# Kernel optimization log

Measured on AMD Instinct MI355X. Metric: run time of the kernel, lower is better.

Reference implementation:

```python
import jax, jax.numpy as jnp
import numpy as np

B, S, DIM = 1, 2048, 2048
NH, NKV, HD = 32, 8, 64
NREP = NH // NKV
SCALE = 1.0 / float(np.sqrt(HD))
NEG = -1e30


def _apply_rope(q, k, rope_cache):
    # q: (B,S,NH,HD), k: (B,S,NKV,HD); rope_cache: (S, HD) = [cos | sin], each HD//2 wide
    cos = rope_cache[:, : HD // 2][None, :, None, :]  # (1,S,1,HD/2)
    sin = rope_cache[:, HD // 2 :][None, :, None, :]

    def rot(x):
        x1, x2 = x[..., : HD // 2], x[..., HD // 2 :]
        return jnp.concatenate([x1 * cos - x2 * sin, x1 * sin + x2 * cos], axis=-1)

    return rot(q), rot(k)


def setup_inputs() -> dict:
    key = jax.random.key(0)
    ks = jax.random.split(key, 12)
    std = 0.02
    x = jax.random.normal(ks[0], (B, S, DIM), jnp.float32)
    # real rotary cos/sin cache
    inv_freq = 1.0 / (10000.0 ** (np.arange(0, HD, 2, dtype=np.float64) / HD))
    freqs = np.outer(np.arange(S, dtype=np.float64), inv_freq)
    rope_cache = jnp.asarray(
        np.concatenate([np.cos(freqs), np.sin(freqs)], axis=-1), jnp.float32
    )  # (S, HD)
    return {
        "x": x,
        "rope_cache": rope_cache,
        "wq_w": jax.random.normal(ks[1], (NH * HD, DIM), jnp.float32) * std,
        "wq_b": jax.random.normal(ks[2], (NH * HD,), jnp.float32) * std,
        "wk_w": jax.random.normal(ks[3], (NKV * HD, DIM), jnp.float32) * std,
        "wk_b": jax.random.normal(ks[4], (NKV * HD,), jnp.float32) * std,
        "wv_w": jax.random.normal(ks[5], (NKV * HD, DIM), jnp.float32) * std,
        "wv_b": jax.random.normal(ks[6], (NKV * HD,), jnp.float32) * std,
        "wo_w": jax.random.normal(ks[7], (DIM, NH * HD), jnp.float32) * std,
        "wo_b": jax.random.normal(ks[8], (DIM,), jnp.float32) * std,
        "sinks": jax.random.normal(ks[9], (NH,), jnp.float32) * std,
    }


def reference(x, rope_cache, wq_w, wq_b, wk_w, wk_b, wv_w, wv_b, wo_w, wo_b, sinks):
    q = (x @ wq_w.T + wq_b).reshape(B, S, NH, HD)
    k = (x @ wk_w.T + wk_b).reshape(B, S, NKV, HD)
    v = (x @ wv_w.T + wv_b).reshape(B, S, NKV, HD)
    q, k = _apply_rope(q, k, rope_cache)
    q = q.transpose(0, 2, 1, 3)  # (B,NH,S,HD)
    k = jnp.repeat(k.transpose(0, 2, 1, 3), NREP, axis=1)  # GQA expand -> (B,NH,S,HD)
    v = jnp.repeat(v.transpose(0, 2, 1, 3), NREP, axis=1)
    scores = jnp.einsum("bhqd,bhkd->bhqk", q, k) * SCALE
    causal = jnp.tril(jnp.ones((S, S), bool))
    scores = jnp.where(causal[None, None], scores, NEG)
    lse = jax.scipy.special.logsumexp(scores, axis=-1)  # (B,NH,S)
    attn = jnp.exp(scores - lse[..., None])
    out = jnp.einsum("bhqk,bhkd->bhqd", attn, v)
    sink_scale = jax.nn.sigmoid(lse - sinks[None, :, None])  # (B,NH,S)
    out = out * sink_scale[..., None]
    out = out.transpose(0, 2, 1, 3).reshape(B, S, NH * HD)
    return out @ wo_w.T + wo_b
```

## Files before the change

kernel.cpp:

```cpp
#include <hip/hip_runtime.h>

typedef unsigned short ushort_t;
typedef short s8v __attribute__((ext_vector_type(8)));
typedef float f4v __attribute__((ext_vector_type(4)));

#define DIMK   2048
#define NHEAD  32
#define HDIM   64
#define SCALE_LOG2E 0.18033688f

__device__ __forceinline__ unsigned short f2bf(float f) {
    unsigned u = __float_as_uint(f);
    u += 0x7fffu + ((u >> 16) & 1u);
    return (unsigned short)(u >> 16);
}

__device__ __forceinline__ unsigned pack_bf2(float f0, float f1) {
    unsigned a = __float_as_uint(f0) + 0x8000u;
    unsigned b = __float_as_uint(f1) + 0x8000u;
    return __builtin_amdgcn_perm(b, a, 0x07060302u);
}

__device__ __forceinline__ float fexp2(float x) {
#if __has_builtin(__builtin_amdgcn_exp2f)
    return __builtin_amdgcn_exp2f(x);
#else
    return exp2f(x);
#endif
}

__device__ __forceinline__ void gll16(const void* g, void* l) {
    __builtin_amdgcn_global_load_lds(
        (const __attribute__((address_space(1))) void*)g,
        (__attribute__((address_space(3))) void*)l, 16, 0, 0);
}

__device__ __forceinline__ f4v mfma16(s8v a, s8v b, f4v c) {
    return __builtin_amdgcn_mfma_f32_16x16x32_bf16(a, b, c, 0, 0, 0);
}

__global__ __launch_bounds__(256) void cast_all(
    const float* __restrict__ x,  const float* __restrict__ wq,
    const float* __restrict__ wk, const float* __restrict__ wv,
    const float* __restrict__ wo,
    ushort_t* __restrict__ xb,  ushort_t* __restrict__ wqb,
    ushort_t* __restrict__ wkb, ushort_t* __restrict__ wvb,
    ushort_t* __restrict__ wob)
{
    int i = blockIdx.x * 256 + threadIdx.x;
    const float* src; ushort_t* dst;
    if      (i < 1048576) { src = x;  dst = xb; }
    else if (i < 2097152) { src = wq; dst = wqb; i -= 1048576; }
    else if (i < 2359296) { src = wk; dst = wkb; i -= 2097152; }
    else if (i < 2621440) { src = wv; dst = wvb; i -= 2359296; }
    else                  { src = wo; dst = wob; i -= 2621440; }
    float4 v = ((const float4*)src)[i];
    ushort4 o;
    o.x = f2bf(v.x); o.y = f2bf(v.y); o.z = f2bf(v.z); o.w = f2bf(v.w);
    ((ushort4*)dst)[i] = o;
}

__device__ __forceinline__ void gemm_core64(
    const ushort_t* __restrict__ A, const ushort_t* __restrict__ Bt,
    int bm, int bn64, ushort_t* As, ushort_t* Bs, f4v acc[2][4])
{
    const int tid  = threadIdx.x;
    const int wave = tid >> 6, lane = tid & 63;
    const int c = lane & 15, q4 = lane >> 4;

    const ushort_t* ag = A  + (size_t)(bm * 128 + wave * 32 + (lane >> 2)) * DIMK + (lane & 3) * 8;
    const ushort_t* bg = Bt + (size_t)(bn64 * 64 + wave * 16 + (lane >> 2)) * DIMK + (lane & 3) * 8;
    ushort_t* as0 = As + (wave * 32) * 32;
    ushort_t* as1 = As + (wave * 32 + 16) * 32;
    ushort_t* bs0 = Bs + (wave * 16) * 32;

    for (int k0 = 0; k0 < DIMK; k0 += 32) {
        gll16(ag + k0,             as0);
        gll16(ag + 16 * DIMK + k0, as1);
        gll16(bg + k0,             bs0);
        __syncthreads();
        s8v af[2], bfv[4];
#pragma unroll
        for (int mt = 0; mt < 2; ++mt)
            af[mt] = *(const s8v*)(As + (wave * 32 + mt * 16 + c) * 32 + q4 * 8);
#pragma unroll
        for (int nt = 0; nt < 4; ++nt)
            bfv[nt] = *(const s8v*)(Bs + (nt * 16 + c) * 32 + q4 * 8);
#pragma unroll
        for (int mt = 0; mt < 2; ++mt)
#pragma unroll
            for (int nt = 0; nt < 4; ++nt)
                acc[mt][nt] = mfma16(af[mt], bfv[nt], acc[mt][nt]);
        __syncthreads();
    }
}

__global__ __launch_bounds__(256) void qkv_gemm(
    const ushort_t* __restrict__ Xb,
    const ushort_t* __restrict__ Wqb, const ushort_t* __restrict__ Wkb, const ushort_t* __restrict__ Wvb,
    const float* __restrict__ biasq, const float* __restrict__ biask, const float* __restrict__ biasv,
    const float* __restrict__ rope,
    ushort_t* __restrict__ Qo, ushort_t* __restrict__ Kblk, ushort_t* __restrict__ Vblk)
{
    __shared__ ushort_t As[128 * 32], Bs[64 * 32];
    const int nb = blockIdx.x, bm = blockIdx.y;
    const ushort_t* Bt; const float* bias; int nbl, mode;
    if      (nb < 32) { Bt = Wqb; bias = biasq; nbl = nb;      mode = 0; }
    else if (nb < 40) { Bt = Wkb; bias = biask; nbl = nb - 32; mode = 1; }
    else              { Bt = Wvb; bias = biasv; nbl = nb - 40; mode = 2; }

    const f4v fz = {0.f, 0.f, 0.f, 0.f};
    f4v acc[2][4];
    for (int i = 0; i < 2; ++i) for (int j = 0; j < 4; ++j) acc[i][j] = fz;

    gemm_core64(Xb, Bt, bm, nbl, As, Bs, acc);

    const int tid = threadIdx.x, wave = tid >> 6, lane = tid & 63;
    const int c = lane & 15, q4 = lane >> 4;

    if (mode == 0) {
#pragma unroll
        for (int mt = 0; mt < 2; ++mt)
#pragma unroll
            for (int r = 0; r < 4; ++r) {
                int row = bm * 128 + wave * 32 + mt * 16 + q4 * 4 + r;
                const float* rp = rope + row * 64;
#pragma unroll
                for (int nt = 0; nt < 2; ++nt) {
                    int d   = nt * 16 + c;
                    int col = nbl * 64 + d;
                    float cs = rp[d], sn = rp[32 + d];
                    float x1 = acc[mt][nt][r]     + bias[col];
                    float x2 = acc[mt][nt + 2][r] + bias[col + 32];
                    Qo[(size_t)row * 2048 + col]      = f2bf((x1 * cs - x2 * sn) * SCALE_LOG2E);
                    Qo[(size_t)row * 2048 + col + 32] = f2bf((x1 * sn + x2 * cs) * SCALE_LOG2E);
                }
            }
    } else if (mode == 1) {
#pragma unroll
        for (int mt = 0; mt < 2; ++mt)
#pragma unroll
            for (int r = 0; r < 4; ++r) {
                int row = bm * 128 + wave * 32 + mt * 16 + q4 * 4 + r;
                const float* rp = rope + row * 64;
                int kt = row >> 6, ntk = (row & 63) >> 4, ck = row & 15;
#pragma unroll
                for (int nt = 0; nt < 2; ++nt) {
                    int d   = nt * 16 + c;
                    int col = nbl * 64 + d;
                    float cs = rp[d], sn = rp[32 + d];
                    float x1 = acc[mt][nt][r]     + bias[col];
                    float x2 = acc[mt][nt + 2][r] + bias[col + 32];
                    float o1 = x1 * cs - x2 * sn;
                    float o2 = x1 * sn + x2 * cs;
                    {   int dd = d;       int kc = dd >> 5, q4k = (dd >> 3) & 3, j = dd & 7;
                        Kblk[(((((size_t)nbl * 32 + kt) * 2 + kc) * 4 + ntk) * 64 + q4k * 16 + ck) * 8 + j] = f2bf(o1); }
                    {   int dd = d + 32;  int kc = dd >> 5, q4k = (dd >> 3) & 3, j = dd & 7;
                        Kblk[(((((size_t)nbl * 32 + kt) * 2 + kc) * 4 + ntk) * 64 + q4k * 16 + ck) * 8 + j] = f2bf(o2); }
                }
            }
    } else {
#pragma unroll
        for (int mt = 0; mt < 2; ++mt)
#pragma unroll
            for (int nt = 0; nt < 4; ++nt)
#pragma unroll
                for (int r = 0; r < 4; ++r) {
                    int row = bm * 128 + wave * 32 + mt * 16 + q4 * 4 + r;
                    int col = nbl * 64 + nt * 16 + c;
                    int kt = row >> 6, K64 = row & 63;
                    int kp = (K64 & 15) * 4 + (K64 >> 4);
                    int kc = kp >> 5, q4v = (kp >> 3) & 3, j = kp & 7;
                    Vblk[(((((size_t)nbl * 32 + kt) * 2 + kc) * 4 + nt) * 64 + q4v * 16 + c) * 8 + j]
                        = f2bf(acc[mt][nt][r] + bias[col]);
                }
    }
}

__global__ __launch_bounds__(256) void proj_gemm(
    const ushort_t* __restrict__ Ob, const ushort_t* __restrict__ Wob,
    const float* __restrict__ bias, float* __restrict__ Co)
{
    __shared__ ushort_t As[128 * 32], Bs[64 * 32];
    const f4v fz = {0.f, 0.f, 0.f, 0.f};
    f4v acc[2][4];
    for (int i = 0; i < 2; ++i) for (int j = 0; j < 4; ++j) acc[i][j] = fz;

    gemm_core64(Ob, Wob, blockIdx.y, blockIdx.x, As, Bs, acc);

    const int tid = threadIdx.x, wave = tid >> 6, lane = tid & 63;
    const int c = lane & 15, q4 = lane >> 4;
#pragma unroll
    for (int mt = 0; mt < 2; ++mt)
#pragma unroll
        for (int nt = 0; nt < 4; ++nt)
#pragma unroll
            for (int r = 0; r < 4; ++r) {
                int row = blockIdx.y * 128 + wave * 32 + mt * 16 + q4 * 4 + r;
                int col = blockIdx.x * 64 + nt * 16 + c;
                Co[(size_t)row * 2048 + col] = acc[mt][nt][r] + bias[col];
            }
}

__global__ __launch_bounds__(256) void attn_kernel(
    const ushort_t* __restrict__ Qb,
    const ushort_t* __restrict__ Kblk,
    const ushort_t* __restrict__ Vblk,
    const float* __restrict__ sinks,
    ushort_t* __restrict__ Ob)
{
    __shared__ ushort_t Ps[4][32 * 72];
    const int p = blockIdx.x, h = blockIdx.y, kvh = h >> 2;
    const int tid = threadIdx.x, wave = tid >> 6, lane = tid & 63;
    const int c = lane & 15, q4 = lane >> 4;
    const int t  = (wave < 2) ? p : (31 - p);
    const int q0 = t * 64 + (wave & 1) * 32;
    ushort_t* Pw = &Ps[wave][0];

    s8v qf[2][2];
#pragma unroll
    for (int mi = 0; mi < 2; ++mi)
#pragma unroll
        for (int kc = 0; kc < 2; ++kc)
            qf[mi][kc] = *(const s8v*)(Qb + (size_t)(q0 + mi * 16 + c) * 2048 + h * 64 + kc * 32 + q4 * 8);

    const f4v fz = {0.f, 0.f, 0.f, 0.f};
    f4v Oacc[2][4];
    float Lp[2][4];
#pragma unroll
    for (int mi = 0; mi < 2; ++mi) {
#pragma unroll
        for (int dt = 0; dt < 4; ++dt) Oacc[mi][dt] = fz;
#pragma unroll
        for (int r = 0; r < 4; ++r) Lp[mi][r] = 0.f;
    }

    const ushort_t* kbase = Kblk + (size_t)kvh * 32 * 4096;
    const ushort_t* vbase = Vblk + (size_t)kvh * 32 * 4096;

    s8v kfA[4][2], vfA[4][2], kfB[4][2], vfB[4][2];

#define ATTN_PF(KF, VF, KT)                                                      \
    do {                                                                         \
        const ushort_t* kp_ = kbase + (size_t)(KT) * 4096;                       \
        const ushort_t* vp_ = vbase + (size_t)(KT) * 4096;                       \
        _Pragma("unroll")                                                        \
        for (int kc = 0; kc < 2; ++kc) {                                         \
            _Pragma("unroll")                                                    \
            for (int nt = 0; nt < 4; ++nt) {                                     \
                KF[nt][kc] = *(const s8v*)(kp_ + ((kc * 4 + nt) * 64 + lane) * 8);\
                VF[nt][kc] = *(const s8v*)(vp_ + ((kc * 4 + nt) * 64 + lane) * 8);\
            }                                                                    \
        }                                                                        \
    } while (0)

#define ATTN_BODY(KF, VF, KT)                                                    \
    do {                                                                         \
        f4v S[2][4];                                                             \
        _Pragma("unroll")                                                        \
        for (int mi = 0; mi < 2; ++mi) {                                         \
            _Pragma("unroll")                                                    \
            for (int nt = 0; nt < 4; ++nt) S[mi][nt] = fz;                       \
        }                                                                        \
        _Pragma("unroll")                                                        \
        for (int kc = 0; kc < 2; ++kc) {                                         \
            _Pragma("unroll")                                                    \
            for (int nt = 0; nt < 4; ++nt) {                                     \
                _Pragma("unroll")                                                \
                for (int mi = 0; mi < 2; ++mi)                                   \
                    S[mi][nt] = mfma16(qf[mi][kc], KF[nt][kc], S[mi][nt]);       \
            }                                                                    \
        }                                                                        \
        if ((KT) == t) {                                                         \
            _Pragma("unroll")                                                    \
            for (int mi = 0; mi < 2; ++mi) {                                     \
                _Pragma("unroll")                                                \
                for (int nt = 0; nt < 4; ++nt) {                                 \
                    int key = t * 64 + nt * 16 + c;                              \
                    _Pragma("unroll")                                            \
                    for (int r = 0; r < 4; ++r) {                                \
                        int qrow = q0 + mi * 16 + q4 * 4 + r;                    \
                        if (key > qrow) S[mi][nt][r] = -1.0e30f;                 \
                    }                                                            \
                }                                                                \
            }                                                                    \
        }                                                                        \
        _Pragma("unroll")                                                        \
        for (int mi = 0; mi < 2; ++mi) {                                         \
            _Pragma("unroll")                                                    \
            for (int r = 0; r < 4; ++r) {                                        \
                float p0 = fexp2(S[mi][0][r]), p1 = fexp2(S[mi][1][r]);          \
                float p2 = fexp2(S[mi][2][r]), p3 = fexp2(S[mi][3][r]);          \
                Lp[mi][r] += (p0 + p1) + (p2 + p3);                              \
                int2 w_; w_.x = (int)pack_bf2(p0, p1); w_.y = (int)pack_bf2(p2, p3); \
                *(int2*)(Pw + (mi * 16 + q4 * 4 + r) * 72 + c * 4) = w_;         \
            }                                                                    \
        }                                                                        \
        s8v pa[2][2];                                                            \
        _Pragma("unroll")                                                        \
        for (int mi = 0; mi < 2; ++mi) {                                         \
            _Pragma("unroll")                                                    \
            for (int kc = 0; kc < 2; ++kc)                                       \
                pa[mi][kc] = *(const s8v*)(Pw + (mi * 16 + c) * 72 + kc * 32 + q4 * 8); \
        }                                                                        \
        _Pragma("unroll")                                                        \
        for (int kc = 0; kc < 2; ++kc) {                                         \
            _Pragma("unroll")                                                    \
            for (int dt = 0; dt < 4; ++dt) {                                     \
                _Pragma("unroll")                                                \
                for (int mi = 0; mi < 2; ++mi)                                   \
                    Oacc[mi][dt] = mfma16(pa[mi][kc], VF[dt][kc], Oacc[mi][dt]); \
            }                                                                    \
        }                                                                        \
    } while (0)

    ATTN_PF(kfA, vfA, 0);
    int kt = 0;
    while (true) {
        int n1 = (kt + 1 <= t) ? kt + 1 : t;
        ATTN_PF(kfB, vfB, n1);
        ATTN_BODY(kfA, vfA, kt);
        ++kt; if (kt > t) break;
        int n2 = (kt + 1 <= t) ? kt + 1 : t;
        ATTN_PF(kfA, vfA, n2);
        ATTN_BODY(kfB, vfB, kt);
        ++kt; if (kt > t) break;
    }
#undef ATTN_PF
#undef ATTN_BODY

#pragma unroll
    for (int mi = 0; mi < 2; ++mi)
#pragma unroll
        for (int r = 0; r < 4; ++r)
#pragma unroll
            for (int off = 1; off < 16; off <<= 1)
                Lp[mi][r] += __shfl_xor(Lp[mi][r], off);

    const float sk = sinks[h];
#pragma unroll
    for (int mi = 0; mi < 2; ++mi)
#pragma unroll
        for (int r = 0; r < 4; ++r) {
            float L = Lp[mi][r];
            float lse = __logf(L);
            float sig = 1.f / (1.f + __expf(sk - lse));
            float sc  = sig / L;
            int row = q0 + mi * 16 + q4 * 4 + r;
#pragma unroll
            for (int dt = 0; dt < 4; ++dt)
                Ob[(size_t)row * 2048 + h * 64 + dt * 16 + c] = f2bf(Oacc[mi][dt][r] * sc);
        }
}

extern "C" void kernel_launch(void* const* d_in, const int* in_sizes, int n_in,
                              void* d_out, int out_size, void* d_ws, size_t ws_size,
                              hipStream_t stream)
{
    (void)in_sizes; (void)n_in; (void)out_size; (void)ws_size;
    const float* x     = (const float*)d_in[0];
    const float* rope  = (const float*)d_in[1];
    const float* wq    = (const float*)d_in[2];
    const float* qb    = (const float*)d_in[3];
    const float* wk    = (const float*)d_in[4];
    const float* kb    = (const float*)d_in[5];
    const float* wv    = (const float*)d_in[6];
    const float* vb    = (const float*)d_in[7];
    const float* wo    = (const float*)d_in[8];
    const float* wob_f = (const float*)d_in[9];
    const float* sinks = (const float*)d_in[10];
    float* out = (float*)d_out;

    char* ws = (char*)d_ws;
    ushort_t* xb   = (ushort_t*)(ws);
    ushort_t* wqb  = (ushort_t*)(ws + (8ull  << 20));
    ushort_t* wkb  = (ushort_t*)(ws + (16ull << 20));
    ushort_t* wvb  = (ushort_t*)(ws + (18ull << 20));
    ushort_t* wob  = (ushort_t*)(ws + (20ull << 20));
    ushort_t* qo   = (ushort_t*)(ws + (28ull << 20));
    ushort_t* kblk = (ushort_t*)(ws + (36ull << 20));
    ushort_t* vblk = (ushort_t*)(ws + (38ull << 20));
    ushort_t* ao   = (ushort_t*)(ws + (40ull << 20));

    cast_all<<<14336, 256, 0, stream>>>(x, wq, wk, wv, wo, xb, wqb, wkb, wvb, wob);
    qkv_gemm<<<dim3(48, 16), 256, 0, stream>>>(xb, wqb, wkb, wvb, qb, kb, vb, rope, qo, kblk, vblk);
    attn_kernel<<<dim3(16, 32), 256, 0, stream>>>(qo, kblk, vblk, sinks, ao);
    proj_gemm<<<dim3(32, 16), 256, 0, stream>>>(ao, wob, wob_f, out);
}
```

Before: 258.5 us.

## Split attention into one 64-row query tile per block with 16-row waves

The attention kernel now launches one block per 64-row query tile (32x32 grid, heaviest tiles first) instead of pairing a light and a heavy tile per block. Each wave now owns 16 query rows instead of 32. The explicit double-buffered K/V register prefetch is replaced by a simple loop that loads K/V each iteration. This gives more blocks and lower register use per wave, aiming for better occupancy and load balance. In exchange, K/V fragments are reused across fewer query rows, so K/V traffic per query rises and latency hiding now depends on occupancy rather than the software prefetch.

New measurement: 265.0 us. +2.5%, slower.

```diff
diff --git a/kernel.cpp b/kernel.cpp
--- a/kernel.cpp
+++ b/kernel.cpp
@@ -209,148 +209,99 @@
     const float* __restrict__ sinks,
     ushort_t* __restrict__ Ob)
 {
-    __shared__ ushort_t Ps[4][32 * 72];
-    const int p = blockIdx.x, h = blockIdx.y, kvh = h >> 2;
+    __shared__ ushort_t Ps[4][16 * 72];
+    const int t = 31 - blockIdx.x, h = blockIdx.y, kvh = h >> 2;
     const int tid = threadIdx.x, wave = tid >> 6, lane = tid & 63;
     const int c = lane & 15, q4 = lane >> 4;
-    const int t  = (wave < 2) ? p : (31 - p);
-    const int q0 = t * 64 + (wave & 1) * 32;
+    const int q0 = t * 64 + wave * 16;
     ushort_t* Pw = &Ps[wave][0];
 
-    s8v qf[2][2];
-#pragma unroll
-    for (int mi = 0; mi < 2; ++mi)
-#pragma unroll
-        for (int kc = 0; kc < 2; ++kc)
-            qf[mi][kc] = *(const s8v*)(Qb + (size_t)(q0 + mi * 16 + c) * 2048 + h * 64 + kc * 32 + q4 * 8);
+    s8v qf[2];
+#pragma unroll
+    for (int kc = 0; kc < 2; ++kc)
+        qf[kc] = *(const s8v*)(Qb + (size_t)(q0 + c) * 2048 + h * 64 + kc * 32 + q4 * 8);
 
     const f4v fz = {0.f, 0.f, 0.f, 0.f};
-    f4v Oacc[2][4];
-    float Lp[2][4];
-#pragma unroll
-    for (int mi = 0; mi < 2; ++mi) {
-#pragma unroll
-        for (int dt = 0; dt < 4; ++dt) Oacc[mi][dt] = fz;
-#pragma unroll
-        for (int r = 0; r < 4; ++r) Lp[mi][r] = 0.f;
-    }
+    f4v Oacc[4];
+    float Lp[4];
+#pragma unroll
+    for (int dt = 0; dt < 4; ++dt) Oacc[dt] = fz;
+#pragma unroll
+    for (int r = 0; r < 4; ++r) Lp[r] = 0.f;
 
     const ushort_t* kbase = Kblk + (size_t)kvh * 32 * 4096;
     const ushort_t* vbase = Vblk + (size_t)kvh * 32 * 4096;
 
-    s8v kfA[4][2], vfA[4][2], kfB[4][2], vfB[4][2];
-
-#define ATTN_PF(KF, VF, KT)                                                      \
-    do {                                                                         \
-        const ushort_t* kp_ = kbase + (size_t)(KT) * 4096;                       \
-        const ushort_t* vp_ = vbase + (size_t)(KT) * 4096;                       \
-        _Pragma("unroll")                                                        \
-        for (int kc = 0; kc < 2; ++kc) {                                         \
-            _Pragma("unroll")                                                    \
-            for (int nt = 0; nt < 4; ++nt) {                                     \
-                KF[nt][kc] = *(const s8v*)(kp_ + ((kc * 4 + nt) * 64 + lane) * 8);\
-                VF[nt][kc] = *(const s8v*)(vp_ + ((kc * 4 + nt) * 64 + lane) * 8);\
-            }                                                                    \
-        }                                                                        \
-    } while (0)
-
-#define ATTN_BODY(KF, VF, KT)                                                    \
-    do {                                                                         \
-        f4v S[2][4];                                                             \
-        _Pragma("unroll")                                                        \
-        for (int mi = 0; mi < 2; ++mi) {                                         \
-            _Pragma("unroll")                                                    \
-            for (int nt = 0; nt < 4; ++nt) S[mi][nt] = fz;                       \
-        }                                                                        \
-        _Pragma("unroll")                                                        \
-        for (int kc = 0; kc < 2; ++kc) {                                         \
-            _Pragma("unroll")                                                    \
-            for (int nt = 0; nt < 4; ++nt) {                                     \
-                _Pragma("unroll")                                                \
-                for (int mi = 0; mi < 2; ++mi)                                   \
-                    S[mi][nt] = mfma16(qf[mi][kc], KF[nt][kc], S[mi][nt]);       \
-            }                                                                    \
-        }                                                                        \
-        if ((KT) == t) {                                                         \
-            _Pragma("unroll")                                                    \
-            for (int mi = 0; mi < 2; ++mi) {                                     \
-                _Pragma("unroll")                                                \
-                for (int nt = 0; nt < 4; ++nt) {                                 \
-                    int key = t * 64 + nt * 16 + c;                              \
-                    _Pragma("unroll")                                            \
-                    for (int r = 0; r < 4; ++r) {                                \
-                        int qrow = q0 + mi * 16 + q4 * 4 + r;                    \
-                        if (key > qrow) S[mi][nt][r] = -1.0e30f;                 \
-                    }                                                            \
-                }                                                                \
-            }                                                                    \
-        }                                                                        \
-        _Pragma("unroll")                                                        \
-        for (int mi = 0; mi < 2; ++mi) {                                         \
-            _Pragma("unroll")                                                    \
-            for (int r = 0; r < 4; ++r) {                                        \
-                float p0 = fexp2(S[mi][0][r]), p1 = fexp2(S[mi][1][r]);          \
-                float p2 = fexp2(S[mi][2][r]), p3 = fexp2(S[mi][3][r]);          \
-                Lp[mi][r] += (p0 + p1) + (p2 + p3);                              \
-                int2 w_; w_.x = (int)pack_bf2(p0, p1); w_.y = (int)pack_bf2(p2, p3); \
-                *(int2*)(Pw + (mi * 16 + q4 * 4 + r) * 72 + c * 4) = w_;         \
-            }                                                                    \
-        }                                                                        \
-        s8v pa[2][2];                                                            \
-        _Pragma("unroll")                                                        \
-        for (int mi = 0; mi < 2; ++mi) {                                         \
-            _Pragma("unroll")                                                    \
-            for (int kc = 0; kc < 2; ++kc)                                       \
-                pa[mi][kc] = *(const s8v*)(Pw + (mi * 16 + c) * 72 + kc * 32 + q4 * 8); \
-        }                                                                        \
-        _Pragma("unroll")                                                        \
-        for (int kc = 0; kc < 2; ++kc) {                                         \
-            _Pragma("unroll")                                                    \
-            for (int dt = 0; dt < 4; ++dt) {                                     \
-                _Pragma("unroll")                                                \
-                for (int mi = 0; mi < 2; ++mi)                                   \
-                    Oacc[mi][dt] = mfma16(pa[mi][kc], VF[dt][kc], Oacc[mi][dt]); \
-            }                                                                    \
-        }                                                                        \
-    } while (0)
-
-    ATTN_PF(kfA, vfA, 0);
-    int kt = 0;
-    while (true) {
-        int n1 = (kt + 1 <= t) ? kt + 1 : t;
-        ATTN_PF(kfB, vfB, n1);
-        ATTN_BODY(kfA, vfA, kt);
-        ++kt; if (kt > t) break;
-        int n2 = (kt + 1 <= t) ? kt + 1 : t;
-        ATTN_PF(kfA, vfA, n2);
-        ATTN_BODY(kfB, vfB, kt);
-        ++kt; if (kt > t) break;
+    for (int kt = 0; kt <= t; ++kt) {
+        const ushort_t* kp = kbase + (size_t)kt * 4096;
+        const ushort_t* vp = vbase + (size_t)kt * 4096;
+        s8v kf[4][2], vf[4][2];
+#pragma unroll
+        for (int kc = 0; kc < 2; ++kc)
+#pragma unroll
+            for (int nt = 0; nt < 4; ++nt) {
+                kf[nt][kc] = *(const s8v*)(kp + ((kc * 4 + nt) * 64 + lane) * 8);
+                vf[nt][kc] = *(const s8v*)(vp + ((kc * 4 + nt) * 64 + lane) * 8);
+            }
+
+        f4v S[4];
+#pragma unroll
+        for (int nt = 0; nt < 4; ++nt) S[nt] = fz;
+#pragma unroll
+        for (int kc = 0; kc < 2; ++kc)
+#pragma unroll
+            for (int nt = 0; nt < 4; ++nt)
+                S[nt] = mfma16(qf[kc], kf[nt][kc], S[nt]);
+
+        if (kt == t) {
+#pragma unroll
+            for (int nt = 0; nt < 4; ++nt) {
+                int key = t * 64 + nt * 16 + c;
+#pragma unroll
+                for (int r = 0; r < 4; ++r) {
+                    int qrow = q0 + q4 * 4 + r;
+                    if (key > qrow) S[nt][r] = -1.0e30f;
+                }
+            }
+        }
+
+#pragma unroll
+        for (int r = 0; r < 4; ++r) {
+            float p0 = fexp2(S[0][r]), p1 = fexp2(S[1][r]);
+            float p2 = fexp2(S[2][r]), p3 = fexp2(S[3][r]);
+            Lp[r] += (p0 + p1) + (p2 + p3);
+            int2 w_; w_.x = (int)pack_bf2(p0, p1); w_.y = (int)pack_bf2(p2, p3);
+            *(int2*)(Pw + (q4 * 4 + r) * 72 + c * 4) = w_;
+        }
+        s8v pa[2];
+#pragma unroll
+        for (int kc = 0; kc < 2; ++kc)
+            pa[kc] = *(const s8v*)(Pw + c * 72 + kc * 32 + q4 * 8);
+#pragma unroll
+        for (int kc = 0; kc < 2; ++kc)
+#pragma unroll
+            for (int dt = 0; dt < 4; ++dt)
+                Oacc[dt] = mfma16(pa[kc], vf[dt][kc], Oacc[dt]);
     }
-#undef ATTN_PF
-#undef ATTN_BODY
-
-#pragma unroll
-    for (int mi = 0; mi < 2; ++mi)
-#pragma unroll
-        for (int r = 0; r < 4; ++r)
-#pragma unroll
-            for (int off = 1; off < 16; off <<= 1)
-                Lp[mi][r] += __shfl_xor(Lp[mi][r], off);
+
+#pragma unroll
+    for (int r = 0; r < 4; ++r)
+#pragma unroll
+        for (int off = 1; off < 16; off <<= 1)
+            Lp[r] += __shfl_xor(Lp[r], off);
 
     const float sk = sinks[h];
 #pragma unroll
-    for (int mi = 0; mi < 2; ++mi)
-#pragma unroll
-        for (int r = 0; r < 4; ++r) {
-            float L = Lp[mi][r];
-            float lse = __logf(L);
-            float sig = 1.f / (1.f + __expf(sk - lse));
-            float sc  = sig / L;
-            int row = q0 + mi * 16 + q4 * 4 + r;
-#pragma unroll
-            for (int dt = 0; dt < 4; ++dt)
-                Ob[(size_t)row * 2048 + h * 64 + dt * 16 + c] = f2bf(Oacc[mi][dt][r] * sc);
-        }
+    for (int r = 0; r < 4; ++r) {
+        float L = Lp[r];
+        float lse = __logf(L);
+        float sig = 1.f / (1.f + __expf(sk - lse));
+        float sc  = sig / L;
+        int row = q0 + q4 * 4 + r;
+#pragma unroll
+        for (int dt = 0; dt < 4; ++dt)
+            Ob[(size_t)row * 2048 + h * 64 + dt * 16 + c] = f2bf(Oacc[dt][r] * sc);
+    }
 }
 
 extern "C" void kernel_launch(void* const* d_in, const int* in_sizes, int n_in,
@@ -384,6 +335,6 @@
 
     cast_all<<<14336, 256, 0, stream>>>(x, wq, wk, wv, wo, xb, wqb, wkb, wvb, wob);
     qkv_gemm<<<dim3(48, 16), 256, 0, stream>>>(xb, wqb, wkb, wvb, qb, kb, vb, rope, qo, kblk, vblk);
-    attn_kernel<<<dim3(16, 32), 256, 0, stream>>>(qo, kblk, vblk, sinks, ao);
+    attn_kernel<<<dim3(32, 32), 256, 0, stream>>>(qo, kblk, vblk, sinks, ao);
     proj_gemm<<<dim3(32, 16), 256, 0, stream>>>(ao, wob, wob_f, out);
 }
```
